# Optimization experiments

Measured on AMD Instinct MI355X. Metric: run time of the kernel, lower is better.

Reference implementation:

```python
import jax, jax.numpy as jnp
import numpy as np

NUM_ITERS = 3


def squash(s, axis=-1):
    # v = (|s|^2 / (1+|s|^2)) * s / |s|
    sq = jnp.sum(s * s, axis=axis, keepdims=True)
    return sq / (1.0 + sq) * s / jnp.sqrt(sq)


def setup_inputs() -> dict:
    key = jax.random.key(0)
    k1, k2 = jax.random.split(key)
    B, C, R, I, O = 256, 10, 1152, 8, 16
    x = jax.random.normal(k1, (B, R, I), dtype=jnp.float32)
    route_weights = jax.random.normal(k2, (C, R, I, O), dtype=jnp.float32)
    return {"x": x, "route_weights": route_weights}


def reference(x, route_weights):
    # x: [B, R, I]; route_weights: [C, R, I, O]
    # u: predictions from each route node for each output capsule: [B, C, R, 1, O]
    u = jnp.einsum("bri,crio->bcro", x, route_weights)[:, :, :, None, :]
    b = jnp.zeros_like(u)
    v = None
    for i in range(NUM_ITERS):
        c = jax.nn.softmax(b, axis=2)          # softmax over route nodes (dim=2)
        s = jnp.sum(c * u, axis=2, keepdims=True)  # [B, C, 1, 1, O]
        v = squash(s, axis=-1)
        if i != NUM_ITERS - 1:
            b = b + jnp.sum(u * v, axis=-1, keepdims=True)  # agreement, broadcast over O
    return v  # [B, C, 1, 1, O]
```

## Files before the change

### kernel.cpp

```cpp
#include <hip/hip_runtime.h>
#include <stdint.h>


#define B_ 256
#define C_ 10
#define R_ 1152
#define I_ 8
#define O_ 16
#define T_ 512
#define KPT 9
#define NW 8
#define NITER 3

typedef float f32x4 __attribute__((ext_vector_type(4)));

__device__ __forceinline__ uint32_t bf16_rn(float f) {
    uint32_t u = __builtin_bit_cast(uint32_t, f);
    return (u + 0x7FFFu + ((u >> 16) & 1u)) >> 16;
}
__device__ __forceinline__ uint32_t pack2(float lo, float hi) {
    return bf16_rn(lo) | (bf16_rn(hi) << 16);
}
__device__ __forceinline__ float unlo(uint32_t p) {
    return __builtin_bit_cast(float, p << 16);
}
__device__ __forceinline__ float unhi(uint32_t p) {
    return __builtin_bit_cast(float, p & 0xFFFF0000u);
}

__global__ __launch_bounds__(T_, 3) void caps_u_kernel(
    const float* __restrict__ x,
    const float* __restrict__ w,
    uint4* __restrict__ u)
{
    const int bx  = blockIdx.x;
    const int c   = bx / 288;
    const int kc  = (bx % 288) >> 5;
    const int bt  = bx & 31;
    const int b0  = bt * 8;
    const int tid = threadIdx.x;
    const int oq  = tid & 3;
    const int rl  = tid >> 2;
    const int r   = kc * 128 + rl;

    __shared__ float xs[8 * 1024];

    {
        const float* xg = x + (size_t)b0 * (R_ * I_) + kc * 1024;
        #pragma unroll
        for (int j = 0; j < 8; ++j) {
            const int e  = j * 512 + tid;
            const int bb = e >> 8;
            const int q  = e & 255;
            const float4 v = *(const float4*)(xg + (size_t)bb * (R_ * I_) + q * 4);
            *(float4*)&xs[e * 4] = v;
        }
    }

    const float* wbase = w + ((size_t)c * R_ + r) * (I_ * O_) + oq * 4;
    f32x4 W0, W1, W2, W3, W4, W5, W6, W7;
    asm volatile("global_load_dwordx4 %0, %1, off"            : "=v"(W0) : "v"(wbase));
    asm volatile("global_load_dwordx4 %0, %1, off offset:64"  : "=v"(W1) : "v"(wbase));
    asm volatile("global_load_dwordx4 %0, %1, off offset:128" : "=v"(W2) : "v"(wbase));
    asm volatile("global_load_dwordx4 %0, %1, off offset:192" : "=v"(W3) : "v"(wbase));
    asm volatile("global_load_dwordx4 %0, %1, off offset:256" : "=v"(W4) : "v"(wbase));
    asm volatile("global_load_dwordx4 %0, %1, off offset:320" : "=v"(W5) : "v"(wbase));
    asm volatile("global_load_dwordx4 %0, %1, off offset:384" : "=v"(W6) : "v"(wbase));
    asm volatile("global_load_dwordx4 %0, %1, off offset:448" : "=v"(W7) : "v"(wbase));
    asm volatile("s_waitcnt vmcnt(0)"
                 : "+v"(W0), "+v"(W1), "+v"(W2), "+v"(W3),
                   "+v"(W4), "+v"(W5), "+v"(W6), "+v"(W7));

    __syncthreads();

    const size_t ubase = (((size_t)(bt * 4) * C_ + c) * KPT + kc) * T_ + tid;

    #pragma unroll
    for (int p = 0; p < 4; ++p) {
        uint32_t lo0, lo1, hi0, hi1;
        #pragma unroll
        for (int h = 0; h < 2; ++h) {
            const int bb = p * 2 + h;
            const float4 xa = *(const float4*)&xs[(bb * 128 + rl) * 8];
            const float4 xb = *(const float4*)&xs[(bb * 128 + rl) * 8 + 4];
            float a0, a1, a2, a3;
            a0 = xa.x * W0[0]; a1 = xa.x * W0[1]; a2 = xa.x * W0[2]; a3 = xa.x * W0[3];
            a0 += xa.y * W1[0]; a1 += xa.y * W1[1]; a2 += xa.y * W1[2]; a3 += xa.y * W1[3];
            a0 += xa.z * W2[0]; a1 += xa.z * W2[1]; a2 += xa.z * W2[2]; a3 += xa.z * W2[3];
            a0 += xa.w * W3[0]; a1 += xa.w * W3[1]; a2 += xa.w * W3[2]; a3 += xa.w * W3[3];
            a0 += xb.x * W4[0]; a1 += xb.x * W4[1]; a2 += xb.x * W4[2]; a3 += xb.x * W4[3];
            a0 += xb.y * W5[0]; a1 += xb.y * W5[1]; a2 += xb.y * W5[2]; a3 += xb.y * W5[3];
            a0 += xb.z * W6[0]; a1 += xb.z * W6[1]; a2 += xb.z * W6[2]; a3 += xb.z * W6[3];
            a0 += xb.w * W7[0]; a1 += xb.w * W7[1]; a2 += xb.w * W7[2]; a3 += xb.w * W7[3];
            if (h == 0) { lo0 = pack2(a0, a1); lo1 = pack2(a2, a3); }
            else        { hi0 = pack2(a0, a1); hi1 = pack2(a2, a3); }
        }
        u[ubase + (size_t)p * (C_ * KPT * T_)] = make_uint4(lo0, lo1, hi0, hi1);
    }
}

__global__ __launch_bounds__(T_, 3) void caps_route_kernel(
    const uint4* __restrict__ u,
    float* __restrict__ out)
{
    const int wg2  = blockIdx.x;
    const int b2   = wg2 / C_;
    const int c    = wg2 % C_;
    const int tid  = threadIdx.x;
    const int lane = tid & 63;
    const int wid  = tid >> 6;
    const int oq   = tid & 3;

    __shared__ float sred[2][NW][4][4];
    __shared__ float zred[2][NW];
    __shared__ float vsum[2][O_];

    uint4 up[KPT];
    #pragma unroll
    for (int k = 0; k < KPT; ++k)
        up[k] = u[((size_t)wg2 * KPT + k) * T_ + tid];

    if (tid < 2 * O_) vsum[tid >> 4][tid & 15] = 0.f;
    __syncthreads();

    #pragma unroll
    for (int it = 0; it < NITER; ++it) {
        float4 vs0 = make_float4(0.f, 0.f, 0.f, 0.f);
        float4 vs1 = vs0;
        if (it > 0) {
            vs0 = *(const float4*)&vsum[0][oq * 4];
            vs1 = *(const float4*)&vsum[1][oq * 4];
        }
        float z0 = 0.f, s00 = 0.f, s01 = 0.f, s02 = 0.f, s03 = 0.f;
        float z1 = 0.f, s10 = 0.f, s11 = 0.f, s12 = 0.f, s13 = 0.f;
        #pragma unroll
        for (int k = 0; k < KPT; ++k) {
            const float u00 = unlo(up[k].x), u01 = unhi(up[k].x);
            const float u02 = unlo(up[k].y), u03 = unhi(up[k].y);
            const float u10 = unlo(up[k].z), u11 = unhi(up[k].z);
            const float u12 = unlo(up[k].w), u13 = unhi(up[k].w);
            float e0, e1;
            if (it == 0) {
                e0 = 1.f; e1 = 1.f;
            } else {
                float d0 = u00 * vs0.x + u01 * vs0.y + u02 * vs0.z + u03 * vs0.w;
                float d1 = u10 * vs1.x + u11 * vs1.y + u12 * vs1.z + u13 * vs1.w;
                d0 += __shfl_xor(d0, 1); d1 += __shfl_xor(d1, 1);
                d0 += __shfl_xor(d0, 2); d1 += __shfl_xor(d1, 2);
                e0 = __expf(d0); e1 = __expf(d1);
            }
            z0 += e0; s00 += e0 * u00; s01 += e0 * u01; s02 += e0 * u02; s03 += e0 * u03;
            z1 += e1; s10 += e1 * u10; s11 += e1 * u11; s12 += e1 * u12; s13 += e1 * u13;
        }
        #pragma unroll
        for (int off = 4; off <= 32; off <<= 1) {
            z0 += __shfl_xor(z0, off);   z1 += __shfl_xor(z1, off);
            s00 += __shfl_xor(s00, off); s01 += __shfl_xor(s01, off);
            s02 += __shfl_xor(s02, off); s03 += __shfl_xor(s03, off);
            s10 += __shfl_xor(s10, off); s11 += __shfl_xor(s11, off);
            s12 += __shfl_xor(s12, off); s13 += __shfl_xor(s13, off);
        }
        if (lane < 4) {
            sred[0][wid][lane][0] = s00; sred[0][wid][lane][1] = s01;
            sred[0][wid][lane][2] = s02; sred[0][wid][lane][3] = s03;
            sred[1][wid][lane][0] = s10; sred[1][wid][lane][1] = s11;
            sred[1][wid][lane][2] = s12; sred[1][wid][lane][3] = s13;
            if (lane == 0) { zred[0][wid] = z0; zred[1][wid] = z1; }
        }
        __syncthreads();

        if (wid == 0 && lane < 2 * O_) {
            const int bb = lane >> 4;
            const int o  = lane & 15;
            float S = 0.f, Z = 0.f;
            #pragma unroll
            for (int wv = 0; wv < NW; ++wv) {
                S += sred[bb][wv][o >> 2][o & 3];
                Z += zred[bb][wv];
            }
            const float inv = 1.f / Z;
            const float svn = S * inv;
            float p = svn * svn;
            p += __shfl_xor(p, 1);
            p += __shfl_xor(p, 2);
            p += __shfl_xor(p, 4);
            p += __shfl_xor(p, 8);
            const float scale = sqrtf(p) / (1.f + p);
            const float vf = svn * scale;
            vsum[bb][o] += vf;
            if (it == NITER - 1)
                out[((size_t)(b2 * 2 + bb) * C_ + c) * O_ + o] = vf;
        }
        if (it != NITER - 1) __syncthreads();
    }
}

#define BPB 4
#define RPP 128

__global__ __launch_bounds__(T_, 2) void capsule_fused_kernel(
    const float* __restrict__ x,
    const float* __restrict__ w,
    float* __restrict__ out)
{
    const int wg   = blockIdx.x;
    const int c    = wg >> 6;
    const int b0   = (wg & 63) * BPB;
    const int tid  = threadIdx.x;
    const int lane = tid & 63;
    const int wid  = tid >> 6;
    const int oq   = tid & 3;
    const int rl   = tid >> 2;

    __shared__ float sred[BPB][NW][4][4];
    __shared__ float zred[BPB][NW];
    __shared__ float vsum[BPB][O_];

    uint32_t up[BPB][KPT][2];

    if (tid < BPB * O_) vsum[tid >> 4][tid & 15] = 0.f;

    #pragma unroll
    for (int k = 0; k < KPT; ++k) {
        const int r = k * RPP + rl;
        const float4* wb4 = (const float4*)(w + ((size_t)c * R_ + r) * (I_ * O_));
        float4 W0 = wb4[0 * 4 + oq], W1 = wb4[1 * 4 + oq];
        float4 W2 = wb4[2 * 4 + oq], W3 = wb4[3 * 4 + oq];
        float4 W4 = wb4[4 * 4 + oq], W5 = wb4[5 * 4 + oq];
        float4 W6 = wb4[6 * 4 + oq], W7 = wb4[7 * 4 + oq];
        #pragma unroll
        for (int bb = 0; bb < BPB; ++bb) {
            const float4* xp = (const float4*)(x + ((size_t)(b0 + bb) * R_ + r) * I_);
            const float4 xa = xp[0];
            const float4 xb = xp[1];
            float a0, a1, a2, a3;
            a0 = xa.x * W0.x; a1 = xa.x * W0.y; a2 = xa.x * W0.z; a3 = xa.x * W0.w;
            a0 += xa.y * W1.x; a1 += xa.y * W1.y; a2 += xa.y * W1.z; a3 += xa.y * W1.w;
            a0 += xa.z * W2.x; a1 += xa.z * W2.y; a2 += xa.z * W2.z; a3 += xa.z * W2.w;
            a0 += xa.w * W3.x; a1 += xa.w * W3.y; a2 += xa.w * W3.z; a3 += xa.w * W3.w;
            a0 += xb.x * W4.x; a1 += xb.x * W4.y; a2 += xb.x * W4.z; a3 += xb.x * W4.w;
            a0 += xb.y * W5.x; a1 += xb.y * W5.y; a2 += xb.y * W5.z; a3 += xb.y * W5.w;
            a0 += xb.z * W6.x; a1 += xb.z * W6.y; a2 += xb.z * W6.z; a3 += xb.z * W6.w;
            a0 += xb.w * W7.x; a1 += xb.w * W7.y; a2 += xb.w * W7.z; a3 += xb.w * W7.w;
            up[bb][k][0] = pack2(a0, a1);
            up[bb][k][1] = pack2(a2, a3);
        }
    }
    __syncthreads();

    #pragma unroll
    for (int it = 0; it < NITER; ++it) {
        float zz[BPB], ss[BPB][4];
        #pragma unroll
        for (int bb = 0; bb < BPB; ++bb) {
            float4 vs = make_float4(0.f, 0.f, 0.f, 0.f);
            if (it > 0) vs = *(const float4*)&vsum[bb][oq * 4];
            float z = 0.f, s0 = 0.f, s1 = 0.f, s2 = 0.f, s3 = 0.f;
            #pragma unroll
            for (int k = 0; k < KPT; ++k) {
                const float u0 = unlo(up[bb][k][0]);
                const float u1 = unhi(up[bb][k][0]);
                const float u2 = unlo(up[bb][k][1]);
                const float u3 = unhi(up[bb][k][1]);
                float e;
                if (it == 0) {
                    e = 1.f;
                } else {
                    float d = u0 * vs.x + u1 * vs.y + u2 * vs.z + u3 * vs.w;
                    d += __shfl_xor(d, 1);
                    d += __shfl_xor(d, 2);
                    e = __expf(d);
                }
                z += e;
                s0 += e * u0; s1 += e * u1; s2 += e * u2; s3 += e * u3;
            }
            zz[bb] = z;
            ss[bb][0] = s0; ss[bb][1] = s1; ss[bb][2] = s2; ss[bb][3] = s3;
        }
        #pragma unroll
        for (int off = 4; off <= 32; off <<= 1) {
            #pragma unroll
            for (int bb = 0; bb < BPB; ++bb) {
                zz[bb] += __shfl_xor(zz[bb], off);
                ss[bb][0] += __shfl_xor(ss[bb][0], off);
                ss[bb][1] += __shfl_xor(ss[bb][1], off);
                ss[bb][2] += __shfl_xor(ss[bb][2], off);
                ss[bb][3] += __shfl_xor(ss[bb][3], off);
            }
        }
        if (lane < 4) {
            #pragma unroll
            for (int bb = 0; bb < BPB; ++bb) {
                sred[bb][wid][lane][0] = ss[bb][0];
                sred[bb][wid][lane][1] = ss[bb][1];
                sred[bb][wid][lane][2] = ss[bb][2];
                sred[bb][wid][lane][3] = ss[bb][3];
                if (lane == 0) zred[bb][wid] = zz[bb];
            }
        }
        __syncthreads();

        if (wid == 0) {
            const int bb = lane >> 4;
            const int o  = lane & 15;
            float S = 0.f, Z = 0.f;
            #pragma unroll
            for (int wv = 0; wv < NW; ++wv) {
                S += sred[bb][wv][o >> 2][o & 3];
                Z += zred[bb][wv];
            }
            const float inv = 1.f / Z;
            const float svn = S * inv;
            float p = svn * svn;
            p += __shfl_xor(p, 1);
            p += __shfl_xor(p, 2);
            p += __shfl_xor(p, 4);
            p += __shfl_xor(p, 8);
            const float scale = sqrtf(p) / (1.f + p);
            const float vf = svn * scale;
            vsum[bb][o] += vf;
            if (it == NITER - 1)
                out[((size_t)(b0 + bb) * C_ + c) * O_ + o] = vf;
        }
        if (it != NITER - 1) __syncthreads();
    }
}

extern "C" void kernel_launch(void* const* d_in, const int* in_sizes, int n_in,
                              void* d_out, int out_size, void* d_ws, size_t ws_size,
                              hipStream_t stream) {
    const float* x = (const float*)d_in[0];
    const float* w = (const float*)d_in[1];
    float* out = (float*)d_out;

    const size_t u_bytes = (size_t)(B_ / 2) * C_ * KPT * T_ * 16;
    if (ws_size >= u_bytes) {
        uint4* u = (uint4*)d_ws;
        caps_u_kernel<<<dim3(C_ * KPT * 32), dim3(T_), 0, stream>>>(x, w, u);
        caps_route_kernel<<<dim3((B_ / 2) * C_), dim3(T_), 0, stream>>>(u, out);
    } else {
        capsule_fused_kernel<<<dim3(C_ * (B_ / BPB)), dim3(T_), 0, stream>>>(x, w, out);
    }
}
```

Baseline: 67.11 us.

## Load x directly from global, drop LDS staging, use nontemporal u stores/loads

The u-producing kernel no longer stages x tiles in shared memory behind a barrier. Each thread now reads its own x rows directly from global memory, and W is loaded with plain loads instead of inline asm. The intermediate u buffer is written and read with nontemporal hints to avoid polluting caches, and occupancy hint raised to 4 blocks. Risk: direct x reads are strided (each thread reads 32B per batch), possibly less coalesced than the staged copy.

```diff
diff --git a/kernel.cpp b/kernel.cpp
--- a/kernel.cpp
+++ b/kernel.cpp
@@ -12,7 +12,7 @@
 #define NW 8
 #define NITER 3
 
-typedef float f32x4 __attribute__((ext_vector_type(4)));
+typedef unsigned int u32x4 __attribute__((ext_vector_type(4)));
 
 __device__ __forceinline__ uint32_t bf16_rn(float f) {
     uint32_t u = __builtin_bit_cast(uint32_t, f);
@@ -28,10 +28,10 @@
     return __builtin_bit_cast(float, p & 0xFFFF0000u);
 }
 
-__global__ __launch_bounds__(T_, 3) void caps_u_kernel(
+__global__ __launch_bounds__(T_, 4) void caps_u_kernel(
     const float* __restrict__ x,
     const float* __restrict__ w,
-    uint4* __restrict__ u)
+    u32x4* __restrict__ u)
 {
     const int bx  = blockIdx.x;
     const int c   = bx / 288;
@@ -43,64 +43,40 @@
     const int rl  = tid >> 2;
     const int r   = kc * 128 + rl;
 
-    __shared__ float xs[8 * 1024];
-
-    {
-        const float* xg = x + (size_t)b0 * (R_ * I_) + kc * 1024;
-        #pragma unroll
-        for (int j = 0; j < 8; ++j) {
-            const int e  = j * 512 + tid;
-            const int bb = e >> 8;
-            const int q  = e & 255;
-            const float4 v = *(const float4*)(xg + (size_t)bb * (R_ * I_) + q * 4);
-            *(float4*)&xs[e * 4] = v;
-        }
-    }
-
-    const float* wbase = w + ((size_t)c * R_ + r) * (I_ * O_) + oq * 4;
-    f32x4 W0, W1, W2, W3, W4, W5, W6, W7;
-    asm volatile("global_load_dwordx4 %0, %1, off"            : "=v"(W0) : "v"(wbase));
-    asm volatile("global_load_dwordx4 %0, %1, off offset:64"  : "=v"(W1) : "v"(wbase));
-    asm volatile("global_load_dwordx4 %0, %1, off offset:128" : "=v"(W2) : "v"(wbase));
-    asm volatile("global_load_dwordx4 %0, %1, off offset:192" : "=v"(W3) : "v"(wbase));
-    asm volatile("global_load_dwordx4 %0, %1, off offset:256" : "=v"(W4) : "v"(wbase));
-    asm volatile("global_load_dwordx4 %0, %1, off offset:320" : "=v"(W5) : "v"(wbase));
-    asm volatile("global_load_dwordx4 %0, %1, off offset:384" : "=v"(W6) : "v"(wbase));
-    asm volatile("global_load_dwordx4 %0, %1, off offset:448" : "=v"(W7) : "v"(wbase));
-    asm volatile("s_waitcnt vmcnt(0)"
-                 : "+v"(W0), "+v"(W1), "+v"(W2), "+v"(W3),
-                   "+v"(W4), "+v"(W5), "+v"(W6), "+v"(W7));
-
-    __syncthreads();
-
-    const size_t ubase = (((size_t)(bt * 4) * C_ + c) * KPT + kc) * T_ + tid;
+    const float4* wb4 = (const float4*)(w + ((size_t)c * R_ + r) * (I_ * O_));
+    const float4 W0 = wb4[0 * 4 + oq], W1 = wb4[1 * 4 + oq];
+    const float4 W2 = wb4[2 * 4 + oq], W3 = wb4[3 * 4 + oq];
+    const float4 W4 = wb4[4 * 4 + oq], W5 = wb4[5 * 4 + oq];
+    const float4 W6 = wb4[6 * 4 + oq], W7 = wb4[7 * 4 + oq];
 
     #pragma unroll
     for (int p = 0; p < 4; ++p) {
-        uint32_t lo0, lo1, hi0, hi1;
+        u32x4 q;
         #pragma unroll
         for (int h = 0; h < 2; ++h) {
-            const int bb = p * 2 + h;
-            const float4 xa = *(const float4*)&xs[(bb * 128 + rl) * 8];
-            const float4 xb = *(const float4*)&xs[(bb * 128 + rl) * 8 + 4];
+            const int b = b0 + p * 2 + h;
+            const float4* xp = (const float4*)(x + ((size_t)b * R_ + r) * I_);
+            const float4 xa = xp[0];
+            const float4 xb = xp[1];
             float a0, a1, a2, a3;
-            a0 = xa.x * W0[0]; a1 = xa.x * W0[1]; a2 = xa.x * W0[2]; a3 = xa.x * W0[3];
-            a0 += xa.y * W1[0]; a1 += xa.y * W1[1]; a2 += xa.y * W1[2]; a3 += xa.y * W1[3];
-            a0 += xa.z * W2[0]; a1 += xa.z * W2[1]; a2 += xa.z * W2[2]; a3 += xa.z * W2[3];
-            a0 += xa.w * W3[0]; a1 += xa.w * W3[1]; a2 += xa.w * W3[2]; a3 += xa.w * W3[3];
-            a0 += xb.x * W4[0]; a1 += xb.x * W4[1]; a2 += xb.x * W4[2]; a3 += xb.x * W4[3];
-            a0 += xb.y * W5[0]; a1 += xb.y * W5[1]; a2 += xb.y * W5[2]; a3 += xb.y * W5[3];
-            a0 += xb.z * W6[0]; a1 += xb.z * W6[1]; a2 += xb.z * W6[2]; a3 += xb.z * W6[3];
-            a0 += xb.w * W7[0]; a1 += xb.w * W7[1]; a2 += xb.w * W7[2]; a3 += xb.w * W7[3];
-            if (h == 0) { lo0 = pack2(a0, a1); lo1 = pack2(a2, a3); }
-            else        { hi0 = pack2(a0, a1); hi1 = pack2(a2, a3); }
-        }
-        u[ubase + (size_t)p * (C_ * KPT * T_)] = make_uint4(lo0, lo1, hi0, hi1);
+            a0 = xa.x * W0.x; a1 = xa.x * W0.y; a2 = xa.x * W0.z; a3 = xa.x * W0.w;
+            a0 += xa.y * W1.x; a1 += xa.y * W1.y; a2 += xa.y * W1.z; a3 += xa.y * W1.w;
+            a0 += xa.z * W2.x; a1 += xa.z * W2.y; a2 += xa.z * W2.z; a3 += xa.z * W2.w;
+            a0 += xa.w * W3.x; a1 += xa.w * W3.y; a2 += xa.w * W3.z; a3 += xa.w * W3.w;
+            a0 += xb.x * W4.x; a1 += xb.x * W4.y; a2 += xb.x * W4.z; a3 += xb.x * W4.w;
+            a0 += xb.y * W5.x; a1 += xb.y * W5.y; a2 += xb.y * W5.z; a3 += xb.y * W5.w;
+            a0 += xb.z * W6.x; a1 += xb.z * W6.y; a2 += xb.z * W6.z; a3 += xb.z * W6.w;
+            a0 += xb.w * W7.x; a1 += xb.w * W7.y; a2 += xb.w * W7.z; a3 += xb.w * W7.w;
+            q[h * 2 + 0] = pack2(a0, a1);
+            q[h * 2 + 1] = pack2(a2, a3);
+        }
+        const size_t ui = (((size_t)(bt * 4 + p) * C_ + c) * KPT + kc) * T_ + tid;
+        __builtin_nontemporal_store(q, &u[ui]);
     }
 }
 
 __global__ __launch_bounds__(T_, 3) void caps_route_kernel(
-    const uint4* __restrict__ u,
+    const u32x4* __restrict__ u,
     float* __restrict__ out)
 {
     const int wg2  = blockIdx.x;
@@ -115,10 +91,10 @@
     __shared__ float zred[2][NW];
     __shared__ float vsum[2][O_];
 
-    uint4 up[KPT];
+    u32x4 up[KPT];
     #pragma unroll
     for (int k = 0; k < KPT; ++k)
-        up[k] = u[((size_t)wg2 * KPT + k) * T_ + tid];
+        up[k] = __builtin_nontemporal_load(&u[((size_t)wg2 * KPT + k) * T_ + tid]);
 
     if (tid < 2 * O_) vsum[tid >> 4][tid & 15] = 0.f;
     __syncthreads();
@@ -135,10 +111,10 @@
         float z1 = 0.f, s10 = 0.f, s11 = 0.f, s12 = 0.f, s13 = 0.f;
         #pragma unroll
         for (int k = 0; k < KPT; ++k) {
-            const float u00 = unlo(up[k].x), u01 = unhi(up[k].x);
-            const float u02 = unlo(up[k].y), u03 = unhi(up[k].y);
-            const float u10 = unlo(up[k].z), u11 = unhi(up[k].z);
-            const float u12 = unlo(up[k].w), u13 = unhi(up[k].w);
+            const float u00 = unlo(up[k][0]), u01 = unhi(up[k][0]);
+            const float u02 = unlo(up[k][1]), u03 = unhi(up[k][1]);
+            const float u10 = unlo(up[k][2]), u11 = unhi(up[k][2]);
+            const float u12 = unlo(up[k][3]), u13 = unhi(up[k][3]);
             float e0, e1;
             if (it == 0) {
                 e0 = 1.f; e1 = 1.f;
@@ -335,7 +311,7 @@
 
     const size_t u_bytes = (size_t)(B_ / 2) * C_ * KPT * T_ * 16;
     if (ws_size >= u_bytes) {
-        uint4* u = (uint4*)d_ws;
+        u32x4* u = (u32x4*)d_ws;
         caps_u_kernel<<<dim3(C_ * KPT * 32), dim3(T_), 0, stream>>>(x, w, u);
         caps_route_kernel<<<dim3((B_ / 2) * C_), dim3(T_), 0, stream>>>(u, out);
     } else {
```

New measurement: 61.26 us. 8.7% less time.
